# Performance work log

Measured on AMD Instinct MI355X. Metric: run time of the kernel, lower is better.

The kernel has to match this reference:

```python
import jax, jax.numpy as jnp
import numpy as np

B, C, D, H, W = 4096, 128, 9, 8, 8  # batch, in_dims, d_emb, fmap_size, fmap_size
EPS = 1e-10


def setup_inputs() -> dict:
    key = jax.random.key(0)
    k1, k2 = jax.random.split(key)
    fcn_activations = jax.random.normal(k1, (B, C, H, W), dtype=jnp.float32)
    # precomputed spatial kernel buffer (emb2 in the torch module): [1, out_dims, H, W]
    emb2 = jax.random.normal(k2, (1, C * D, H, W), dtype=jnp.float32)
    return {"fcn_activations": fcn_activations, "emb2": emb2}


def reference(fcn_activations, emb2):
    b, c, h, w = fcn_activations.shape
    d = emb2.shape[1] // c  # d_emb
    # idx1 = arange(c*d)//d, i.e. channel i is repeated d times consecutively.
    # gather + elementwise mult + spatial sum == contraction below (no big emb1 intermediate):
    kern = emb2.reshape(c, d, h, w)
    out = jnp.einsum('bchw,cdhw->bcd', fcn_activations, kern).reshape(b, c * d)
    # L2Norm over last dim
    norm = jnp.sqrt(jnp.sum(out * out, axis=-1) + EPS)
    return out / norm[:, None]
```

## Files before the change

kernel.cpp:

```cpp
#include <hip/hip_runtime.h>


constexpr int B_TOT = 4096;
constexpr int C_CH  = 128;
constexpr int D_EMB = 9;
constexpr int THREADS = 256;
constexpr int GPB = 32;
constexpr int NCH = 4;
constexpr int RB  = 8;

__device__ __forceinline__ float reduce8_hw(float p) {
    p += __int_as_float(__builtin_amdgcn_mov_dpp(__float_as_int(p), 0xB1,  0xf, 0xf, true));
    p += __int_as_float(__builtin_amdgcn_mov_dpp(__float_as_int(p), 0x4E,  0xf, 0xf, true));
    p += __int_as_float(__builtin_amdgcn_mov_dpp(__float_as_int(p), 0x141, 0xf, 0xf, true));
    return p;
}

__global__ __launch_bounds__(THREADS, 2)
void esenc_fused(const float* __restrict__ fcn,
                 const float* __restrict__ kern,
                 float* __restrict__ out) {
    __shared__ float red[4 * RB];
    __shared__ float invn[RB];

    const int tid = threadIdx.x;
    const int l   = tid & 7;
    const int g   = tid >> 3;
    const int w   = tid >> 6;
    const int b0  = blockIdx.x * RB;

    const float4* kern4 = (const float4*)kern;
    const float4* f4    = (const float4*)fcn;

    float keep[NCH][D_EMB];

#pragma unroll
    for (int ch = 0; ch < NCH; ++ch) {
        const int c = ch * GPB + g;

        float4 k0[D_EMB], k1[D_EMB];
#pragma unroll
        for (int d = 0; d < D_EMB; ++d) {
            const unsigned kb = (unsigned)(c * D_EMB + d) * 16u;
            k0[d] = kern4[kb + l];
            k1[d] = kern4[kb + 8u + l];
        }

        const unsigned fb = ((unsigned)b0 * C_CH + (unsigned)c) * 16u;
        float4 a0 = f4[fb + l];
        float4 a1 = f4[fb + 8u + l];

#pragma unroll
        for (int r = 0; r < RB; ++r) {
            const float4 c0 = a0, c1 = a1;
            if (r + 1 < RB) {
                const unsigned fn = fb + (unsigned)(r + 1) * (C_CH * 16u);
                a0 = f4[fn + l];
                a1 = f4[fn + 8u + l];
            }
#pragma unroll
            for (int d = 0; d < D_EMB; ++d) {
                float t;
                t = c0.x * k0[d].x;
                t = fmaf(c0.y, k0[d].y, t);
                t = fmaf(c0.z, k0[d].z, t);
                t = fmaf(c0.w, k0[d].w, t);
                t = fmaf(c1.x, k1[d].x, t);
                t = fmaf(c1.y, k1[d].y, t);
                t = fmaf(c1.z, k1[d].z, t);
                t = fmaf(c1.w, k1[d].w, t);
                t = reduce8_hw(t);
                if (l == r) keep[ch][d] = t;
            }
        }
    }

    float s = 0.0f;
#pragma unroll
    for (int ch = 0; ch < NCH; ++ch)
#pragma unroll
        for (int d = 0; d < D_EMB; ++d)
            s = fmaf(keep[ch][d], keep[ch][d], s);

    s += __shfl_xor(s, 8,  64);
    s += __shfl_xor(s, 16, 64);
    s += __shfl_xor(s, 32, 64);
    if ((tid & 63) < 8) red[w * RB + l] = s;
    __syncthreads();
    if (tid < RB) {
        float t = red[tid] + red[RB + tid] + red[2 * RB + tid] + red[3 * RB + tid];
        invn[tid] = 1.0f / sqrtf(t + 1e-10f);
    }
    __syncthreads();
    const float inv = invn[l];

#pragma unroll
    for (int ch = 0; ch < NCH; ++ch) {
        const int c = ch * GPB + g;
        float* op = out + (size_t)(b0 + l) * (C_CH * D_EMB) + c * D_EMB;
#pragma unroll
        for (int d = 0; d < D_EMB; ++d)
            op[d] = keep[ch][d] * inv;
    }
}

extern "C" void kernel_launch(void* const* d_in, const int* in_sizes, int n_in,
                              void* d_out, int out_size, void* d_ws, size_t ws_size,
                              hipStream_t stream) {
    const float* fcn  = (const float*)d_in[0];
    const float* kern = (const float*)d_in[1];
    float* out = (float*)d_out;

    dim3 grid(B_TOT / RB), block(THREADS);
    hipLaunchKernelGGL(esenc_fused, grid, block, 0, stream, fcn, kern, out);
}
```

Baseline: 35.42 us.

## Double block size and split per-channel work into register-light phases

Raises the block to 512 threads so each thread group covers 2 channels instead of 4. Each channel's 9 embedding dims are split into 5+4 phases separated by scheduling barriers, which lowers peak register use and allows 4 blocks per CU. The activation prefetch across rows is dropped, and activations are now reloaded in each phase. The intent is higher occupancy to hide memory latency, at the cost of redundant activation loads (served from cache) and less ILP.

```diff
diff --git a/kernel.cpp b/kernel.cpp
--- a/kernel.cpp
+++ b/kernel.cpp
@@ -4,9 +4,7 @@
 constexpr int B_TOT = 4096;
 constexpr int C_CH  = 128;
 constexpr int D_EMB = 9;
-constexpr int THREADS = 256;
-constexpr int GPB = 32;
-constexpr int NCH = 4;
+constexpr int THREADS = 512;
 constexpr int RB  = 8;
 
 __device__ __forceinline__ float reduce8_hw(float p) {
@@ -16,91 +14,98 @@
     return p;
 }
 
-__global__ __launch_bounds__(THREADS, 2)
+__device__ __forceinline__ float dot8(const float4& a0, const float4& a1,
+                                      const float4& b0, const float4& b1) {
+    float t;
+    t = a0.x * b0.x;
+    t = fmaf(a0.y, b0.y, t);
+    t = fmaf(a0.z, b0.z, t);
+    t = fmaf(a0.w, b0.w, t);
+    t = fmaf(a1.x, b1.x, t);
+    t = fmaf(a1.y, b1.y, t);
+    t = fmaf(a1.z, b1.z, t);
+    t = fmaf(a1.w, b1.w, t);
+    return t;
+}
+
+template<int D0, int ND>
+__device__ __forceinline__ void phase(unsigned c, int l, unsigned b0,
+                                      const float4* __restrict__ f4,
+                                      const float4* __restrict__ kern4,
+                                      float keep[D_EMB]) {
+    float4 k0[ND], k1[ND];
+#pragma unroll
+    for (int d = 0; d < ND; ++d) {
+        const unsigned kb = (c * D_EMB + (unsigned)(D0 + d)) * 16u;
+        k0[d] = kern4[kb + l];
+        k1[d] = kern4[kb + 8u + l];
+    }
+#pragma unroll
+    for (int r = 0; r < RB; ++r) {
+        const unsigned fb = ((b0 + (unsigned)r) * C_CH + c) * 16u;
+        const float4 a0 = f4[fb + l];
+        const float4 a1 = f4[fb + 8u + l];
+#pragma unroll
+        for (int d = 0; d < ND; ++d) {
+            float t = dot8(a0, a1, k0[d], k1[d]);
+            t = reduce8_hw(t);
+            if (l == r) keep[D0 + d] = t;
+        }
+    }
+}
+
+__global__ __launch_bounds__(THREADS, 4)
 void esenc_fused(const float* __restrict__ fcn,
                  const float* __restrict__ kern,
                  float* __restrict__ out) {
-    __shared__ float red[4 * RB];
+    __shared__ float red[8 * RB];
     __shared__ float invn[RB];
 
     const int tid = threadIdx.x;
     const int l   = tid & 7;
     const int g   = tid >> 3;
     const int w   = tid >> 6;
-    const int b0  = blockIdx.x * RB;
+    const unsigned b0 = blockIdx.x * RB;
 
     const float4* kern4 = (const float4*)kern;
     const float4* f4    = (const float4*)fcn;
 
-    float keep[NCH][D_EMB];
+    float keepA[D_EMB], keepB[D_EMB];
 
-#pragma unroll
-    for (int ch = 0; ch < NCH; ++ch) {
-        const int c = ch * GPB + g;
-
-        float4 k0[D_EMB], k1[D_EMB];
-#pragma unroll
-        for (int d = 0; d < D_EMB; ++d) {
-            const unsigned kb = (unsigned)(c * D_EMB + d) * 16u;
-            k0[d] = kern4[kb + l];
-            k1[d] = kern4[kb + 8u + l];
-        }
-
-        const unsigned fb = ((unsigned)b0 * C_CH + (unsigned)c) * 16u;
-        float4 a0 = f4[fb + l];
-        float4 a1 = f4[fb + 8u + l];
-
-#pragma unroll
-        for (int r = 0; r < RB; ++r) {
-            const float4 c0 = a0, c1 = a1;
-            if (r + 1 < RB) {
-                const unsigned fn = fb + (unsigned)(r + 1) * (C_CH * 16u);
-                a0 = f4[fn + l];
-                a1 = f4[fn + 8u + l];
-            }
-#pragma unroll
-            for (int d = 0; d < D_EMB; ++d) {
-                float t;
-                t = c0.x * k0[d].x;
-                t = fmaf(c0.y, k0[d].y, t);
-                t = fmaf(c0.z, k0[d].z, t);
-                t = fmaf(c0.w, k0[d].w, t);
-                t = fmaf(c1.x, k1[d].x, t);
-                t = fmaf(c1.y, k1[d].y, t);
-                t = fmaf(c1.z, k1[d].z, t);
-                t = fmaf(c1.w, k1[d].w, t);
-                t = reduce8_hw(t);
-                if (l == r) keep[ch][d] = t;
-            }
-        }
-    }
+    phase<0, 5>((unsigned)g, l, b0, f4, kern4, keepA);
+    __builtin_amdgcn_sched_barrier(0);
+    phase<5, 4>((unsigned)g, l, b0, f4, kern4, keepA);
+    __builtin_amdgcn_sched_barrier(0);
+    phase<0, 5>((unsigned)(64 + g), l, b0, f4, kern4, keepB);
+    __builtin_amdgcn_sched_barrier(0);
+    phase<5, 4>((unsigned)(64 + g), l, b0, f4, kern4, keepB);
 
     float s = 0.0f;
 #pragma unroll
-    for (int ch = 0; ch < NCH; ++ch)
-#pragma unroll
-        for (int d = 0; d < D_EMB; ++d)
-            s = fmaf(keep[ch][d], keep[ch][d], s);
-
+    for (int d = 0; d < D_EMB; ++d) {
+        s = fmaf(keepA[d], keepA[d], s);
+        s = fmaf(keepB[d], keepB[d], s);
+    }
     s += __shfl_xor(s, 8,  64);
     s += __shfl_xor(s, 16, 64);
     s += __shfl_xor(s, 32, 64);
     if ((tid & 63) < 8) red[w * RB + l] = s;
     __syncthreads();
     if (tid < RB) {
-        float t = red[tid] + red[RB + tid] + red[2 * RB + tid] + red[3 * RB + tid];
+        float t = 0.0f;
+#pragma unroll
+        for (int j = 0; j < 8; ++j) t += red[j * RB + tid];
         invn[tid] = 1.0f / sqrtf(t + 1e-10f);
     }
     __syncthreads();
     const float inv = invn[l];
 
+    float* opA = out + (size_t)(b0 + l) * (C_CH * D_EMB) + g * D_EMB;
+    float* opB = opA + 64 * D_EMB;
 #pragma unroll
-    for (int ch = 0; ch < NCH; ++ch) {
-        const int c = ch * GPB + g;
-        float* op = out + (size_t)(b0 + l) * (C_CH * D_EMB) + c * D_EMB;
-#pragma unroll
-        for (int d = 0; d < D_EMB; ++d)
-            op[d] = keep[ch][d] * inv;
+    for (int d = 0; d < D_EMB; ++d) {
+        opA[d] = keepA[d] * inv;
+        opB[d] = keepB[d] * inv;
     }
 }
 
```

After: 96.63 us. 173% more time.

## Stage output rows in LDS for coalesced float4 stores and halve rows per block

Applied to the files above, without the earlier changes.

Reduces the rows per block from 8 to 4, which doubles the grid and has each block load the kernel weights once per d instead of keeping all of them in registers. Results are written to a shared-memory tile and then stored as coalesced float4 writes scaled by the inverse norm, replacing the strided scalar stores of 9 floats per thread. The price is that half of the lanes (l>=4) compute dot products that are thrown away, kern is reloaded twice as often across the grid, and there is an extra LDS pass.

```diff
diff --git a/kernel.cpp b/kernel.cpp
--- a/kernel.cpp
+++ b/kernel.cpp
@@ -7,7 +7,8 @@
 constexpr int THREADS = 256;
 constexpr int GPB = 32;
 constexpr int NCH = 4;
-constexpr int RB  = 8;
+constexpr int RB  = 4;
+constexpr int ROWF = C_CH * D_EMB;
 
 __device__ __forceinline__ float reduce8_hw(float p) {
     p += __int_as_float(__builtin_amdgcn_mov_dpp(__float_as_int(p), 0xB1,  0xf, 0xf, true));
@@ -20,6 +21,7 @@
 void esenc_fused(const float* __restrict__ fcn,
                  const float* __restrict__ kern,
                  float* __restrict__ out) {
+    __shared__ __align__(16) float tile[RB * ROWF];
     __shared__ float red[4 * RB];
     __shared__ float invn[RB];
 
@@ -27,48 +29,41 @@
     const int l   = tid & 7;
     const int g   = tid >> 3;
     const int w   = tid >> 6;
-    const int b0  = blockIdx.x * RB;
+    const unsigned b0 = blockIdx.x * RB;
 
     const float4* kern4 = (const float4*)kern;
     const float4* f4    = (const float4*)fcn;
 
-    float keep[NCH][D_EMB];
+    float keep[NCH][D_EMB] = {};
 
 #pragma unroll
     for (int ch = 0; ch < NCH; ++ch) {
-        const int c = ch * GPB + g;
+        const unsigned c = (unsigned)(ch * GPB + g);
 
-        float4 k0[D_EMB], k1[D_EMB];
+        float4 f0[RB], f1[RB];
+#pragma unroll
+        for (int r = 0; r < RB; ++r) {
+            const unsigned fb = ((b0 + (unsigned)r) * C_CH + c) * 16u;
+            f0[r] = f4[fb + l];
+            f1[r] = f4[fb + 8u + l];
+        }
+
 #pragma unroll
         for (int d = 0; d < D_EMB; ++d) {
-            const unsigned kb = (unsigned)(c * D_EMB + d) * 16u;
-            k0[d] = kern4[kb + l];
-            k1[d] = kern4[kb + 8u + l];
-        }
-
-        const unsigned fb = ((unsigned)b0 * C_CH + (unsigned)c) * 16u;
-        float4 a0 = f4[fb + l];
-        float4 a1 = f4[fb + 8u + l];
-
+            const unsigned kb = (c * D_EMB + (unsigned)d) * 16u;
+            const float4 k0 = kern4[kb + l];
+            const float4 k1 = kern4[kb + 8u + l];
 #pragma unroll
-        for (int r = 0; r < RB; ++r) {
-            const float4 c0 = a0, c1 = a1;
-            if (r + 1 < RB) {
-                const unsigned fn = fb + (unsigned)(r + 1) * (C_CH * 16u);
-                a0 = f4[fn + l];
-                a1 = f4[fn + 8u + l];
-            }
-#pragma unroll
-            for (int d = 0; d < D_EMB; ++d) {
+            for (int r = 0; r < RB; ++r) {
                 float t;
-                t = c0.x * k0[d].x;
-                t = fmaf(c0.y, k0[d].y, t);
-                t = fmaf(c0.z, k0[d].z, t);
-                t = fmaf(c0.w, k0[d].w, t);
-                t = fmaf(c1.x, k1[d].x, t);
-                t = fmaf(c1.y, k1[d].y, t);
-                t = fmaf(c1.z, k1[d].z, t);
-                t = fmaf(c1.w, k1[d].w, t);
+                t = f0[r].x * k0.x;
+                t = fmaf(f0[r].y, k0.y, t);
+                t = fmaf(f0[r].z, k0.z, t);
+                t = fmaf(f0[r].w, k0.w, t);
+                t = fmaf(f1[r].x, k1.x, t);
+                t = fmaf(f1[r].y, k1.y, t);
+                t = fmaf(f1[r].z, k1.z, t);
+                t = fmaf(f1[r].w, k1.w, t);
                 t = reduce8_hw(t);
                 if (l == r) keep[ch][d] = t;
             }
@@ -85,22 +80,34 @@
     s += __shfl_xor(s, 8,  64);
     s += __shfl_xor(s, 16, 64);
     s += __shfl_xor(s, 32, 64);
-    if ((tid & 63) < 8) red[w * RB + l] = s;
-    __syncthreads();
-    if (tid < RB) {
-        float t = red[tid] + red[RB + tid] + red[2 * RB + tid] + red[3 * RB + tid];
-        invn[tid] = 1.0f / sqrtf(t + 1e-10f);
+    if ((tid & 63) < RB) red[w * RB + l] = s;
+
+    if (l < RB) {
+#pragma unroll
+        for (int ch = 0; ch < NCH; ++ch) {
+            const int c = ch * GPB + g;
+#pragma unroll
+            for (int d = 0; d < D_EMB; ++d)
+                tile[l * ROWF + c * D_EMB + d] = keep[ch][d];
+        }
     }
     __syncthreads();
-    const float inv = invn[l];
+    if (tid < RB)
+        invn[tid] = 1.0f / sqrtf(red[tid] + red[RB + tid] + red[2 * RB + tid]
+                                 + red[3 * RB + tid] + 1e-10f);
+    __syncthreads();
 
+    const float4* t4 = (const float4*)tile;
+    float4* o4 = (float4*)(out + (size_t)b0 * ROWF);
 #pragma unroll
-    for (int ch = 0; ch < NCH; ++ch) {
-        const int c = ch * GPB + g;
-        float* op = out + (size_t)(b0 + l) * (C_CH * D_EMB) + c * D_EMB;
-#pragma unroll
-        for (int d = 0; d < D_EMB; ++d)
-            op[d] = keep[ch][d] * inv;
+    for (int j = 0; j < (RB * ROWF / 4) / THREADS + 1; ++j) {
+        const int i = tid + j * THREADS;
+        if (i < RB * ROWF / 4) {
+            const float inv = invn[i / (ROWF / 4)];
+            float4 v = t4[i];
+            v.x *= inv; v.y *= inv; v.z *= inv; v.w *= inv;
+            o4[i] = v;
+        }
     }
 }
 
```

Result: faster. 31.53 us (median of 2 runs) (-11.0%).
